# Performance work log

Hardware: AMD Instinct MI355X
Metric: run time of the kernel (lower is better)

The kernel has to match this reference:

```python
import jax, jax.numpy as jnp
import numpy as np

N_NODES = 50000
N_EDGES = 800000
N_GRAPHS = 256
F_IN = 75  # num_features_xd


def _lin_params(key, fan_in, fan_out):
    kw, kb = jax.random.split(key)
    s = 1.0 / np.sqrt(fan_in)
    W = jax.random.uniform(kw, (fan_in, fan_out), jnp.float32, -s, s)
    b = jax.random.uniform(kb, (fan_out,), jnp.float32, -s, s)
    return W, b


def setup_inputs() -> dict:
    key = jax.random.key(0)
    ks = jax.random.split(key, 8)
    x = jax.random.normal(ks[0], (N_NODES, F_IN), jnp.float32)
    edge_index = jax.random.randint(ks[1], (2, N_EDGES), 0, N_NODES, jnp.int32)
    batch = jnp.sort(jax.random.randint(ks[2], (N_NODES,), 0, N_GRAPHS, jnp.int32))
    W1, b1 = _lin_params(ks[3], F_IN, F_IN)            # conv1: 75 -> 75
    W2, b2 = _lin_params(ks[4], F_IN, 2 * F_IN)        # conv2: 75 -> 150
    W3, b3 = _lin_params(ks[5], 2 * F_IN, 4 * F_IN)    # conv3: 150 -> 300
    Wg1, bg1 = _lin_params(ks[6], 4 * F_IN, 1024)      # fc_g1: 300 -> 1024
    Wg2, bg2 = _lin_params(ks[7], 1024, 128)           # fc_g2: 1024 -> 128
    return dict(x=x, edge_index=edge_index, batch=batch,
                W1=W1, b1=b1, W2=W2, b2=b2, W3=W3, b3=b3,
                Wg1=Wg1, bg1=bg1, Wg2=Wg2, bg2=bg2)


def gcn_conv(x, W, b, src, dst, n):
    """PyG GCNConv: out = D^{-1/2}(A+I)D^{-1/2} X W + b (symmetric norm, self loops)."""
    h = x @ W                                   # [n, out]
    loop = jnp.arange(n, dtype=src.dtype)
    s = jnp.concatenate([src, loop])            # [E+n]
    d = jnp.concatenate([dst, loop])
    deg = jax.ops.segment_sum(jnp.ones(s.shape[0], x.dtype), d, num_segments=n)
    dinv = jnp.where(deg > 0, jax.lax.rsqrt(jnp.maximum(deg, 1e-12)), 0.0)
    norm = dinv[s] * dinv[d]                    # [E+n]
    out = jax.ops.segment_sum(norm[:, None] * h[s], d, num_segments=n)
    return out + b


def reference(x, edge_index, batch, W1, b1, W2, b2, W3, b3, Wg1, bg1, Wg2, bg2):
    src, dst = edge_index[0], edge_index[1]
    n = x.shape[0]
    h = jax.nn.relu(gcn_conv(x, W1, b1, src, dst, n))
    h = jax.nn.relu(gcn_conv(h, W2, b2, src, dst, n))
    h = jax.nn.relu(gcn_conv(h, W3, b3, src, dst, n))
    g = jax.ops.segment_max(h, batch, num_segments=N_GRAPHS)  # global max pool
    g = jax.nn.relu(g @ Wg1 + bg1)
    # dropout is identity in eval mode
    return g @ Wg2 + bg2
```

## Files before the change

### kernel.cpp

```cpp
#include <hip/hip_runtime.h>
#include <math.h>

#define SCAN_B 1024

typedef __attribute__((ext_vector_type(8))) short short8v;
typedef __attribute__((ext_vector_type(8))) unsigned short ushort8v;
typedef __attribute__((ext_vector_type(4))) float f32x4;

static inline int ceil_div_i(long long a, int b) { return (int)((a + b - 1) / b); }

__device__ __forceinline__ unsigned short f2bf(float x) {
    unsigned int u = __float_as_uint(x);
    u += 0x7fffu + ((u >> 16) & 1u);
    return (unsigned short)(u >> 16);
}
__device__ __forceinline__ float bf2f(unsigned short h) {
    return __uint_as_float(((unsigned int)h) << 16);
}
__device__ __forceinline__ ushort8v zero8() {
    ushort8v z;
#pragma unroll
    for (int e = 0; e < 8; e++) z[e] = 0;
    return z;
}


__global__ __launch_bounds__(256) void k_count(const int* __restrict__ dst, int E,
                                               int* __restrict__ cnt) {
    int i = blockIdx.x * blockDim.x + threadIdx.x;
    if (i < E) atomicAdd(&cnt[dst[i]], 1);
}

__global__ __launch_bounds__(256) void k_dinv(const int* __restrict__ cnt,
                                              float* __restrict__ dinv, int N) {
    int i = blockIdx.x * blockDim.x + threadIdx.x;
    if (i < N) dinv[i] = (float)(1.0 / sqrt((double)(cnt[i] + 1)));
}

__global__ __launch_bounds__(256) void k_scan1(const int* __restrict__ cnt,
                                               int* __restrict__ rowptr,
                                               int* __restrict__ bsum, int N) {
    __shared__ int s[256];
    int tid = threadIdx.x;
    int base = blockIdx.x * SCAN_B + tid * 4;
    int a0 = (base + 0 < N) ? cnt[base + 0] : 0;
    int a1 = (base + 1 < N) ? cnt[base + 1] : 0;
    int a2 = (base + 2 < N) ? cnt[base + 2] : 0;
    int a3 = (base + 3 < N) ? cnt[base + 3] : 0;
    int tsum = a0 + a1 + a2 + a3;
    s[tid] = tsum;
    __syncthreads();
    for (int off = 1; off < 256; off <<= 1) {
        int val = 0;
        if (tid >= off) val = s[tid - off];
        __syncthreads();
        if (tid >= off) s[tid] += val;
        __syncthreads();
    }
    int texcl = s[tid] - tsum;
    if (tid == 255) bsum[blockIdx.x] = s[255];
    if (base + 0 < N) rowptr[base + 0] = texcl;
    if (base + 1 < N) rowptr[base + 1] = texcl + a0;
    if (base + 2 < N) rowptr[base + 2] = texcl + a0 + a1;
    if (base + 3 < N) rowptr[base + 3] = texcl + a0 + a1 + a2;
}

__global__ __launch_bounds__(256) void k_scan2(int* __restrict__ bsum, int NB) {
    __shared__ int s[256];
    int tid = threadIdx.x;
    int v = (tid < NB) ? bsum[tid] : 0;
    s[tid] = v;
    __syncthreads();
    for (int off = 1; off < 256; off <<= 1) {
        int val = 0;
        if (tid >= off) val = s[tid - off];
        __syncthreads();
        if (tid >= off) s[tid] += val;
        __syncthreads();
    }
    if (tid < NB) bsum[tid] = s[tid] - v;
}

__global__ __launch_bounds__(256) void k_scan3(int* __restrict__ rowptr,
                                               const int* __restrict__ bsum, int N, int E) {
    int i = blockIdx.x * blockDim.x + threadIdx.x;
    if (i < N) rowptr[i] += bsum[i >> 10];
    if (i == 0) rowptr[N] = E;
}

__global__ __launch_bounds__(256) void k_fill(const int* __restrict__ src,
                                              const int* __restrict__ dst, int E,
                                              const int* __restrict__ rowptr,
                                              int* __restrict__ fill,
                                              int* __restrict__ col) {
    int e = blockIdx.x * blockDim.x + threadIdx.x;
    if (e >= E) return;
    int s = src[e], d = dst[e];
    int pos = atomicAdd(&fill[d], 1);
    col[rowptr[d] + pos] = s;
}


__global__ __launch_bounds__(256) void k_xscale(const float* __restrict__ x,
                                                const float* __restrict__ dinv,
                                                unsigned short* __restrict__ xb,
                                                int N, int F, int XS) {
    int i = blockIdx.x * blockDim.x + threadIdx.x;
    int v = i / XS, c = i - v * XS;
    if (v >= N) return;
    float val = (c < F) ? dinv[v] * x[(size_t)v * F + c] : 0.f;
    xb[i] = f2bf(val);
}


template <int CHUNKS, int SLOTS, int UNR>
__global__ __launch_bounds__(256) void k_gather_s(const unsigned short* __restrict__ Xb,
                                                  const int* __restrict__ rowptr,
                                                  const int* __restrict__ col,
                                                  unsigned short* __restrict__ Th,
                                                  unsigned short* __restrict__ Tl,
                                                  int N, int XS, int KPf) {
    const int v = blockIdx.x * 4 + (threadIdx.x >> 6);
    const int lane = threadIdx.x & 63;
    if (v >= N) return;
    constexpr int VW = 8;
    const int slot = lane / CHUNKS;
    const int chunk = lane - slot * CHUNKS;
    const bool act = lane < CHUNKS * SLOTS;
    const int f0 = chunk * VW;

    float acc[VW];
#pragma unroll
    for (int u = 0; u < VW; u++) acc[u] = 0.f;
    if (slot == 0) {
        ushort8v h = *(const ushort8v*)(Xb + (size_t)v * XS + f0);
#pragma unroll
        for (int u = 0; u < VW; u++) acc[u] = bf2f(h[u]);
    }

    const int beg = rowptr[v], end = rowptr[v + 1];
    for (int jb = beg; jb < end; jb += 64) {
        const int nj = min(64, end - jb);
        int ec = 0;
        if (lane < nj) ec = col[jb + lane];
        for (int e = 0; e < nj; e += SLOTS * UNR) {
            int cs[UNR];
            bool vs[UNR];
#pragma unroll
            for (int u = 0; u < UNR; u++) {
                int srcl = e + u * SLOTS + slot;
                vs[u] = act && (srcl < nj);
                cs[u] = __shfl(ec, srcl & 63);
            }
            ushort8v xv[UNR];
#pragma unroll
            for (int u = 0; u < UNR; u++) {
                xv[u] = zero8();
                if (vs[u]) xv[u] = *(const ushort8v*)(Xb + (size_t)cs[u] * XS + f0);
            }
#pragma unroll
            for (int u = 0; u < UNR; u++)
#pragma unroll
                for (int k2 = 0; k2 < VW; k2++)
                    acc[k2] += bf2f(xv[u][k2]);
        }
    }

#pragma unroll
    for (int k2 = 0; k2 < VW; k2++) {
        float t2 = acc[k2];
#pragma unroll
        for (int s2 = 1; s2 < SLOTS; s2++) t2 += __shfl(acc[k2], chunk + s2 * CHUNKS);
        acc[k2] = t2;
    }

    if (slot == 0 && f0 < KPf) {
        ushort8v h8, l8;
#pragma unroll
        for (int u = 0; u < VW; u++) {
            unsigned short hh = f2bf(acc[u]);
            h8[u] = hh;
            l8[u] = f2bf(acc[u] - bf2f(hh));
        }
        *(ushort8v*)(Th + (size_t)v * KPf + f0) = h8;
        *(ushort8v*)(Tl + (size_t)v * KPf + f0) = l8;
    }
}


__global__ __launch_bounds__(256) void k_wsplit(const float* __restrict__ W,
                                                unsigned short* __restrict__ Wth,
                                                unsigned short* __restrict__ Wtl,
                                                int K, int Fout, int KP) {
    int i = blockIdx.x * blockDim.x + threadIdx.x;
    if (i >= Fout * KP) return;
    int c = i / KP, k = i - c * KP;
    float w = (k < K) ? W[(size_t)k * Fout + c] : 0.f;
    unsigned short h = f2bf(w);
    Wth[i] = h;
    Wtl[i] = f2bf(w - bf2f(h));
}


template <int NT, int MODE>
__global__ __launch_bounds__(256) void k_gemm_br(
    const unsigned short* __restrict__ Ah, const unsigned short* __restrict__ Al,
    const unsigned short* __restrict__ Bth, const unsigned short* __restrict__ Btl,
    const float* __restrict__ bias, const float* __restrict__ dinvp,
    unsigned short* __restrict__ Cb, int CSbf,
    const int* __restrict__ batch, float* __restrict__ G,
    int N, int Fout) {
    constexpr int KP = NT * 32;
    constexpr int PL = 8 * NT * 512;
    __shared__ unsigned short sB[2 * PL];
    __shared__ int sBatch[128];

    const int t = threadIdx.x;
    const int r0 = blockIdx.x * 128;
    const int c0 = blockIdx.y * 128;
    const int lane = t & 63;
    const int wv = t >> 6;
    const int l15 = lane & 15;
    const int lg = lane >> 4;

    constexpr int KG = KP >> 3;
    for (int i = t; i < 128 * KG; i += 256) {
        int colc = i / KG, kg = i - colc * KG;
        int gc = c0 + colc;
        ushort8v h = zero8(), l = zero8();
        if (gc < Fout) {
            h = *(const ushort8v*)(Bth + (size_t)gc * KP + kg * 8);
            l = *(const ushort8v*)(Btl + (size_t)gc * KP + kg * 8);
        }
        int jt = colc >> 4, tc = kg >> 2, g = kg & 3;
        int off = (jt * NT + tc) * 512 + ((colc & 15) + 16 * g) * 8;
        *(ushort8v*)&sB[off] = h;
        *(ushort8v*)&sB[PL + off] = l;
    }
    if (MODE == 1 && t < 128) sBatch[t] = (r0 + t < N) ? batch[r0 + t] : -1;
    __syncthreads();

    const int wrow = wv * 32;
    const int row0 = r0 + wrow + l15;
    const int row1 = row0 + 16;
    const bool ok0 = row0 < N;
    const bool ok1 = row1 < N;
    const unsigned short* a0h = Ah + (size_t)row0 * KP;
    const unsigned short* a0l = Al + (size_t)row0 * KP;
    const unsigned short* a1h = Ah + (size_t)row1 * KP;
    const unsigned short* a1l = Al + (size_t)row1 * KP;

    f32x4 acc[2][8];
#pragma unroll
    for (int i = 0; i < 2; i++)
#pragma unroll
        for (int j = 0; j < 8; j++) acc[i][j] = (f32x4){0.f, 0.f, 0.f, 0.f};

#pragma unroll 2
    for (int tc = 0; tc < NT; ++tc) {
        const int ko = tc * 32 + lg * 8;
        short8v A0h = ok0 ? *(const short8v*)(a0h + ko) : (short8v)zero8();
        short8v A0l = ok0 ? *(const short8v*)(a0l + ko) : (short8v)zero8();
        short8v A1h = ok1 ? *(const short8v*)(a1h + ko) : (short8v)zero8();
        short8v A1l = ok1 ? *(const short8v*)(a1l + ko) : (short8v)zero8();
#pragma unroll
        for (int j = 0; j < 8; j++) {
            const int off = (j * NT + tc) * 512 + lane * 8;
            short8v bh = *(const short8v*)&sB[off];
            short8v bl = *(const short8v*)&sB[PL + off];
            acc[0][j] = __builtin_amdgcn_mfma_f32_16x16x32_bf16(A0l, bh, acc[0][j], 0, 0, 0);
            acc[0][j] = __builtin_amdgcn_mfma_f32_16x16x32_bf16(A0h, bl, acc[0][j], 0, 0, 0);
            acc[0][j] = __builtin_amdgcn_mfma_f32_16x16x32_bf16(A0h, bh, acc[0][j], 0, 0, 0);
            acc[1][j] = __builtin_amdgcn_mfma_f32_16x16x32_bf16(A1l, bh, acc[1][j], 0, 0, 0);
            acc[1][j] = __builtin_amdgcn_mfma_f32_16x16x32_bf16(A1h, bl, acc[1][j], 0, 0, 0);
            acc[1][j] = __builtin_amdgcn_mfma_f32_16x16x32_bf16(A1h, bh, acc[1][j], 0, 0, 0);
        }
    }

    float drw[8];
#pragma unroll
    for (int i = 0; i < 2; i++)
#pragma unroll
        for (int q = 0; q < 4; q++) {
            int gr = r0 + wrow + i * 16 + (lane >> 4) * 4 + q;
            drw[i * 4 + q] = (gr < N) ? dinvp[gr] : 0.f;
        }

    if (MODE == 0) {
#pragma unroll
        for (int j = 0; j < 8; j++) {
            int gc = c0 + j * 16 + l15;
            if (gc >= CSbf) continue;
            float bv = (gc < Fout) ? bias[gc] : 0.f;
#pragma unroll
            for (int i = 0; i < 2; i++) {
                int rb = r0 + wrow + i * 16 + (lane >> 4) * 4;
#pragma unroll
                for (int q = 0; q < 4; q++) {
                    int gr = rb + q;
                    if (gr >= N) continue;
                    float dr = drw[i * 4 + q];
                    float vv = (gc < Fout) ? fmaxf(fmaf(acc[i][j][q], dr, bv), 0.f) * dr : 0.f;
                    Cb[(size_t)gr * CSbf + gc] = f2bf(vv);
                }
            }
        }
    } else {
#pragma unroll
        for (int j = 0; j < 8; j++) {
            int gc = c0 + j * 16 + l15;
            if (gc >= Fout) continue;
            float bv = bias[gc];
            int gcur = -1;
            float vmax = 0.f;
#pragma unroll
            for (int i = 0; i < 2; i++) {
                int lr = wrow + i * 16 + (lane >> 4) * 4;
#pragma unroll
                for (int q = 0; q < 4; q++) {
                    int g = sBatch[lr + q];
                    float vv = fmaxf(fmaf(acc[i][j][q], drw[i * 4 + q], bv), 0.f);
                    if (g < 0) continue;
                    if (g != gcur) {
                        if (gcur >= 0)
                            atomicMax((int*)&G[(size_t)gcur * Fout + gc], __float_as_int(vmax));
                        gcur = g;
                        vmax = vv;
                    } else {
                        vmax = fmaxf(vmax, vv);
                    }
                }
            }
            if (gcur >= 0) atomicMax((int*)&G[(size_t)gcur * Fout + gc], __float_as_int(vmax));
        }
    }
}


__global__ __launch_bounds__(256) void k_fc1(const float* __restrict__ A,
                                             const float* __restrict__ W,
                                             const float* __restrict__ bias,
                                             float* __restrict__ C,
                                             int M, int K, int Nout) {
    __shared__ float sA[2 * 304];
    const int t = threadIdx.x;
    const int m0 = blockIdx.x * 2;
    const int oc = blockIdx.y * 256 + t;

    for (int i = t; i < 2 * K; i += 256) {
        int r = i / K, k = i - r * K;
        sA[r * 304 + k] = (m0 + r < M) ? A[(size_t)(m0 + r) * K + k] : 0.f;
    }
    __syncthreads();

    float acc0 = 0.f, acc1 = 0.f;
    int k = 0;
    for (; k + 8 <= K; k += 8) {
        float w[8];
#pragma unroll
        for (int u = 0; u < 8; u++) w[u] = W[(size_t)(k + u) * Nout + oc];
#pragma unroll
        for (int u = 0; u < 8; u++) {
            acc0 = fmaf(sA[k + u], w[u], acc0);
            acc1 = fmaf(sA[304 + k + u], w[u], acc1);
        }
    }
    for (; k < K; k++) {
        float w = W[(size_t)k * Nout + oc];
        acc0 = fmaf(sA[k], w, acc0);
        acc1 = fmaf(sA[304 + k], w, acc1);
    }
    float bv = bias[oc];
    if (m0 < M) C[(size_t)m0 * Nout + oc] = fmaxf(acc0 + bv, 0.f);
    if (m0 + 1 < M) C[(size_t)(m0 + 1) * Nout + oc] = fmaxf(acc1 + bv, 0.f);
}


__global__ __launch_bounds__(256) void k_fc2p(const float* __restrict__ A,
                                              const float* __restrict__ W,
                                              float* __restrict__ P,
                                              int M, int K, int Nout) {
    __shared__ float sA[2 * 256];
    const int t = threadIdx.x;
    const int m0 = blockIdx.x * 2;
    const int sk = blockIdx.y;
    const int k0 = sk * 256;
    const int row = t >> 7;
    const int oc = t & 127;

    for (int i = t; i < 2 * 256; i += 256) {
        int r = i >> 8, k = i & 255;
        sA[i] = (m0 + r < M) ? A[(size_t)(m0 + r) * K + k0 + k] : 0.f;
    }
    __syncthreads();

    const float* a = sA + row * 256;
    float acc = 0.f;
    for (int k = 0; k < 256; k += 8) {
        float w[8];
#pragma unroll
        for (int u = 0; u < 8; u++) w[u] = W[(size_t)(k0 + k + u) * Nout + oc];
#pragma unroll
        for (int u = 0; u < 8; u++) acc = fmaf(a[k + u], w[u], acc);
    }
    int m = m0 + row;
    if (m < M) P[((size_t)sk * M + m) * Nout + oc] = acc;
}

__global__ __launch_bounds__(256) void k_fc2r(const float* __restrict__ P,
                                              const float* __restrict__ bias,
                                              float* __restrict__ C,
                                              int M, int Nout, int SK) {
    int i = blockIdx.x * blockDim.x + threadIdx.x;
    if (i >= M * Nout) return;
    int oc = i % Nout;
    float acc = bias[oc];
    for (int s2 = 0; s2 < SK; s2++) acc += P[(size_t)s2 * M * Nout + i];
    C[i] = acc;
}


extern "C" void kernel_launch(void* const* d_in, const int* in_sizes, int n_in,
                              void* d_out, int out_size, void* d_ws, size_t ws_size,
                              hipStream_t stream) {
    const float* x     = (const float*)d_in[0];
    const int*   ei    = (const int*)d_in[1];
    const int*   batch = (const int*)d_in[2];
    const float* W1 = (const float*)d_in[3];
    const float* b1 = (const float*)d_in[4];
    const float* W2 = (const float*)d_in[5];
    const float* b2 = (const float*)d_in[6];
    const float* W3 = (const float*)d_in[7];
    const float* b3 = (const float*)d_in[8];
    const float* Wg1 = (const float*)d_in[9];
    const float* bg1 = (const float*)d_in[10];
    const float* Wg2 = (const float*)d_in[11];
    const float* bg2 = (const float*)d_in[12];

    const int N  = in_sizes[2];
    const int E  = in_sizes[1] / 2;
    const int F1 = in_sizes[4];
    const int F2 = in_sizes[6];
    const int F3 = in_sizes[8];
    const int H1 = in_sizes[10];
    const int OC = in_sizes[12];
    const int NG = out_size / OC;
    const int FIN = in_sizes[3] / F1;

    const int KP1 = 96;
    const int KP3 = 160;

    const int* src = ei;
    const int* dst = ei + E;

    char* base = (char*)d_ws;
    size_t off = 0;
    auto alloc = [&](size_t bytes) -> void* {
        void* p = base + off;
        off = (off + bytes + 255) & ~(size_t)255;
        return p;
    };
    int*   cnt    = (int*)alloc((size_t)N * 4);
    int*   fill   = (int*)alloc((size_t)N * 4);
    int*   rowptr = (int*)alloc((size_t)(N + 1) * 4);
    float* dinv   = (float*)alloc((size_t)N * 4);
    int*   bsum   = (int*)alloc(256 * 4);
    int*   col    = (int*)alloc((size_t)E * 4);
    unsigned short* W1th = (unsigned short*)alloc((size_t)F1 * KP1 * 2);
    unsigned short* W1tl = (unsigned short*)alloc((size_t)F1 * KP1 * 2);
    unsigned short* W2th = (unsigned short*)alloc((size_t)F2 * KP1 * 2);
    unsigned short* W2tl = (unsigned short*)alloc((size_t)F2 * KP1 * 2);
    unsigned short* W3th = (unsigned short*)alloc((size_t)F3 * KP3 * 2);
    unsigned short* W3tl = (unsigned short*)alloc((size_t)F3 * KP3 * 2);
    float* Gb  = (float*)alloc((size_t)NG * F3 * 4);
    float* g1  = (float*)alloc((size_t)NG * H1 * 4);
    float* P2  = (float*)alloc((size_t)4 * NG * OC * 4);
    unsigned short* TgH = (unsigned short*)alloc((size_t)N * KP3 * 2);
    unsigned short* TgL = (unsigned short*)alloc((size_t)N * KP3 * 2);
    unsigned short* Xb  = (unsigned short*)alloc((size_t)N * KP1 * 2);
    unsigned short* H1b = (unsigned short*)alloc((size_t)N * KP1 * 2);
    unsigned short* H2b = (unsigned short*)alloc((size_t)N * KP3 * 2);

    hipMemsetAsync(cnt, 0, (size_t)N * 4, stream);
    hipMemsetAsync(fill, 0, (size_t)N * 4, stream);
    hipMemsetAsync(Gb, 0, (size_t)NG * F3 * 4, stream);

    k_count<<<ceil_div_i(E, 256), 256, 0, stream>>>(dst, E, cnt);
    k_dinv<<<ceil_div_i(N, 256), 256, 0, stream>>>(cnt, dinv, N);
    int NB = ceil_div_i(N, SCAN_B);
    k_scan1<<<NB, 256, 0, stream>>>(cnt, rowptr, bsum, N);
    k_scan2<<<1, 256, 0, stream>>>(bsum, NB);
    k_scan3<<<ceil_div_i(N, 256), 256, 0, stream>>>(rowptr, bsum, N, E);
    k_fill<<<ceil_div_i(E, 256), 256, 0, stream>>>(src, dst, E, rowptr, fill, col);

    k_wsplit<<<ceil_div_i((long long)F1 * KP1, 256), 256, 0, stream>>>(W1, W1th, W1tl, FIN, F1, KP1);
    k_wsplit<<<ceil_div_i((long long)F2 * KP1, 256), 256, 0, stream>>>(W2, W2th, W2tl, F1, F2, KP1);
    k_wsplit<<<ceil_div_i((long long)F3 * KP3, 256), 256, 0, stream>>>(W3, W3th, W3tl, F2, F3, KP3);
    k_xscale<<<ceil_div_i((long long)N * KP1, 256), 256, 0, stream>>>(x, dinv, Xb, N, FIN, KP1);

    dim3 blk(256);
    int gw = ceil_div_i(N, 4);
    int gx = ceil_div_i(N, 128);

    k_gather_s<12, 5, 2><<<gw, blk, 0, stream>>>(Xb, rowptr, col, TgH, TgL, N, KP1, KP1);
    {
        dim3 g(gx, ceil_div_i(F1, 128));
        k_gemm_br<3, 0><<<g, blk, 0, stream>>>(TgH, TgL, W1th, W1tl, b1, dinv, H1b, KP1,
                                               nullptr, nullptr, N, F1);
    }
    k_gather_s<12, 5, 2><<<gw, blk, 0, stream>>>(H1b, rowptr, col, TgH, TgL, N, KP1, KP1);
    {
        dim3 g(gx, ceil_div_i(F2, 128));
        k_gemm_br<3, 0><<<g, blk, 0, stream>>>(TgH, TgL, W2th, W2tl, b2, dinv, H2b, KP3,
                                               nullptr, nullptr, N, F2);
    }
    k_gather_s<20, 3, 4><<<gw, blk, 0, stream>>>(H2b, rowptr, col, TgH, TgL, N, KP3, KP3);
    {
        dim3 g(gx, ceil_div_i(F3, 128));
        k_gemm_br<5, 1><<<g, blk, 0, stream>>>(TgH, TgL, W3th, W3tl, b3, dinv, nullptr, 0,
                                               batch, Gb, N, F3);
    }

    {
        dim3 g(ceil_div_i(NG, 2), H1 / 256);
        k_fc1<<<g, 256, 0, stream>>>(Gb, Wg1, bg1, g1, NG, F3, H1);
    }
    {
        dim3 g(ceil_div_i(NG, 2), 4);
        k_fc2p<<<g, 256, 0, stream>>>(g1, Wg2, P2, NG, H1, OC);
        k_fc2r<<<ceil_div_i((long long)NG * OC, 256), 256, 0, stream>>>(
            P2, bg2, (float*)d_out, NG, OC, 4);
    }
}
```

Before: 379.2 us.

## Shrink feature strides, use 16-bit column indices, and retile GEMM to exact widths

Stores column indices as 16-bit values and has k_scan3 write the fill cursor directly, which removes a memset and the rowptr lookup in k_fill. k_fill now handles four edges per thread. Intermediate activation buffers move from 96/160-wide padding to 80/152-wide strides, so the gathers move fewer bytes. The GEMM is rewritten to stream B through padded LDS tiles one K-slice at a time, with column tiles sized to the true output widths (96/160), instead of preloading 128-wide tiles. The 16-bit indices only hold while N stays below 65536, and the per-K-slice syncthreads add synchronisation.

```diff
diff --git a/kernel.cpp b/kernel.cpp
--- a/kernel.cpp
+++ b/kernel.cpp
@@ -2,6 +2,7 @@
 #include <math.h>
 
 #define SCAN_B 1024
+#define LDST 40
 
 typedef __attribute__((ext_vector_type(8))) short short8v;
 typedef __attribute__((ext_vector_type(8))) unsigned short ushort8v;
@@ -82,22 +83,31 @@
 }
 
 __global__ __launch_bounds__(256) void k_scan3(int* __restrict__ rowptr,
-                                               const int* __restrict__ bsum, int N, int E) {
+                                               const int* __restrict__ bsum,
+                                               int* __restrict__ fill, int N, int E) {
     int i = blockIdx.x * blockDim.x + threadIdx.x;
-    if (i < N) rowptr[i] += bsum[i >> 10];
+    if (i < N) {
+        int r = rowptr[i] + bsum[i >> 10];
+        rowptr[i] = r;
+        fill[i] = r;
+    }
     if (i == 0) rowptr[N] = E;
 }
 
 __global__ __launch_bounds__(256) void k_fill(const int* __restrict__ src,
                                               const int* __restrict__ dst, int E,
-                                              const int* __restrict__ rowptr,
                                               int* __restrict__ fill,
-                                              int* __restrict__ col) {
-    int e = blockIdx.x * blockDim.x + threadIdx.x;
-    if (e >= E) return;
-    int s = src[e], d = dst[e];
-    int pos = atomicAdd(&fill[d], 1);
-    col[rowptr[d] + pos] = s;
+                                              unsigned short* __restrict__ col) {
+    int base = blockIdx.x * (256 * 4) + threadIdx.x;
+#pragma unroll
+    for (int u = 0; u < 4; u++) {
+        int e = base + u * 256;
+        if (e < E) {
+            int s = src[e], d = dst[e];
+            int idx = atomicAdd(&fill[d], 1);
+            col[idx] = (unsigned short)s;
+        }
+    }
 }
 
 
@@ -116,7 +126,7 @@
 template <int CHUNKS, int SLOTS, int UNR>
 __global__ __launch_bounds__(256) void k_gather_s(const unsigned short* __restrict__ Xb,
                                                   const int* __restrict__ rowptr,
-                                                  const int* __restrict__ col,
+                                                  const unsigned short* __restrict__ col,
                                                   unsigned short* __restrict__ Th,
                                                   unsigned short* __restrict__ Tl,
                                                   int N, int XS, int KPf) {
@@ -142,7 +152,7 @@
     for (int jb = beg; jb < end; jb += 64) {
         const int nj = min(64, end - jb);
         int ec = 0;
-        if (lane < nj) ec = col[jb + lane];
+        if (lane < nj) ec = (int)col[jb + lane];
         for (int e = 0; e < nj; e += SLOTS * UNR) {
             int cs[UNR];
             bool vs[UNR];
@@ -202,72 +212,74 @@
 }
 
 
-template <int NT, int MODE>
-__global__ __launch_bounds__(256) void k_gemm_br(
-    const unsigned short* __restrict__ Ah, const unsigned short* __restrict__ Al,
+template <int NJ2, int MODE>
+__global__ __launch_bounds__(256, 4) void k_gemm_ad(
+    const unsigned short* __restrict__ Ahp, const unsigned short* __restrict__ Alp, int KPf,
     const unsigned short* __restrict__ Bth, const unsigned short* __restrict__ Btl,
     const float* __restrict__ bias, const float* __restrict__ dinvp,
     unsigned short* __restrict__ Cb, int CSbf,
     const int* __restrict__ batch, float* __restrict__ G,
-    int N, int Fout) {
-    constexpr int KP = NT * 32;
-    constexpr int PL = 8 * NT * 512;
-    __shared__ unsigned short sB[2 * PL];
+    int N, int KP, int Fout) {
+    constexpr int CT = 16 * NJ2;
+    __shared__ unsigned short sBh[CT * LDST];
+    __shared__ unsigned short sBl[CT * LDST];
     __shared__ int sBatch[128];
 
     const int t = threadIdx.x;
     const int r0 = blockIdx.x * 128;
-    const int c0 = blockIdx.y * 128;
+    const int c0 = blockIdx.y * CT;
     const int lane = t & 63;
     const int wv = t >> 6;
+    const int wrow = wv * 32;
     const int l15 = lane & 15;
     const int lg = lane >> 4;
-
-    constexpr int KG = KP >> 3;
-    for (int i = t; i < 128 * KG; i += 256) {
-        int colc = i / KG, kg = i - colc * KG;
-        int gc = c0 + colc;
-        ushort8v h = zero8(), l = zero8();
-        if (gc < Fout) {
-            h = *(const ushort8v*)(Bth + (size_t)gc * KP + kg * 8);
-            l = *(const ushort8v*)(Btl + (size_t)gc * KP + kg * 8);
-        }
-        int jt = colc >> 4, tc = kg >> 2, g = kg & 3;
-        int off = (jt * NT + tc) * 512 + ((colc & 15) + 16 * g) * 8;
-        *(ushort8v*)&sB[off] = h;
-        *(ushort8v*)&sB[PL + off] = l;
-    }
+    const int nt = KP >> 5;
+
     if (MODE == 1 && t < 128) sBatch[t] = (r0 + t < N) ? batch[r0 + t] : -1;
-    __syncthreads();
-
-    const int wrow = wv * 32;
+
     const int row0 = r0 + wrow + l15;
     const int row1 = row0 + 16;
     const bool ok0 = row0 < N;
     const bool ok1 = row1 < N;
-    const unsigned short* a0h = Ah + (size_t)row0 * KP;
-    const unsigned short* a0l = Al + (size_t)row0 * KP;
-    const unsigned short* a1h = Ah + (size_t)row1 * KP;
-    const unsigned short* a1l = Al + (size_t)row1 * KP;
-
-    f32x4 acc[2][8];
+    const unsigned short* a0h = Ahp + (size_t)row0 * KPf;
+    const unsigned short* a0l = Alp + (size_t)row0 * KPf;
+    const unsigned short* a1h = Ahp + (size_t)row1 * KPf;
+    const unsigned short* a1l = Alp + (size_t)row1 * KPf;
+
+    f32x4 acc[2][NJ2];
 #pragma unroll
     for (int i = 0; i < 2; i++)
 #pragma unroll
-        for (int j = 0; j < 8; j++) acc[i][j] = (f32x4){0.f, 0.f, 0.f, 0.f};
-
-#pragma unroll 2
-    for (int tc = 0; tc < NT; ++tc) {
-        const int ko = tc * 32 + lg * 8;
-        short8v A0h = ok0 ? *(const short8v*)(a0h + ko) : (short8v)zero8();
-        short8v A0l = ok0 ? *(const short8v*)(a0l + ko) : (short8v)zero8();
-        short8v A1h = ok1 ? *(const short8v*)(a1h + ko) : (short8v)zero8();
-        short8v A1l = ok1 ? *(const short8v*)(a1l + ko) : (short8v)zero8();
-#pragma unroll
-        for (int j = 0; j < 8; j++) {
-            const int off = (j * NT + tc) * 512 + lane * 8;
-            short8v bh = *(const short8v*)&sB[off];
-            short8v bl = *(const short8v*)&sB[PL + off];
+        for (int j = 0; j < NJ2; j++) acc[i][j] = (f32x4){0.f, 0.f, 0.f, 0.f};
+
+    for (int tc = 0; tc < nt; ++tc) {
+        const int kk = tc * 32;
+        for (int idx = t; idx < CT * 4; idx += 256) {
+            int brow = idx >> 2, seg = idx & 3;
+            int gc = c0 + brow;
+            ushort8v h = zero8(), l = zero8();
+            if (gc < Fout) {
+                h = *(const ushort8v*)(Bth + (size_t)gc * KP + kk + seg * 8);
+                l = *(const ushort8v*)(Btl + (size_t)gc * KP + kk + seg * 8);
+            }
+            int boff = brow * LDST + seg * 8;
+            *(ushort8v*)&sBh[boff] = h;
+            *(ushort8v*)&sBl[boff] = l;
+        }
+        __syncthreads();
+
+        const int gk = kk + lg * 8;
+        const bool kok = gk < KPf;
+        short8v A0h = (ok0 && kok) ? *(const short8v*)(a0h + gk) : (short8v)zero8();
+        short8v A0l = (ok0 && kok) ? *(const short8v*)(a0l + gk) : (short8v)zero8();
+        short8v A1h = (ok1 && kok) ? *(const short8v*)(a1h + gk) : (short8v)zero8();
+        short8v A1l = (ok1 && kok) ? *(const short8v*)(a1l + gk) : (short8v)zero8();
+
+#pragma unroll
+        for (int j = 0; j < NJ2; j++) {
+            int co = (j * 16 + l15) * LDST + lg * 8;
+            short8v bh = *(const short8v*)&sBh[co];
+            short8v bl = *(const short8v*)&sBl[co];
             acc[0][j] = __builtin_amdgcn_mfma_f32_16x16x32_bf16(A0l, bh, acc[0][j], 0, 0, 0);
             acc[0][j] = __builtin_amdgcn_mfma_f32_16x16x32_bf16(A0h, bl, acc[0][j], 0, 0, 0);
             acc[0][j] = __builtin_amdgcn_mfma_f32_16x16x32_bf16(A0h, bh, acc[0][j], 0, 0, 0);
@@ -275,6 +287,7 @@
             acc[1][j] = __builtin_amdgcn_mfma_f32_16x16x32_bf16(A1h, bl, acc[1][j], 0, 0, 0);
             acc[1][j] = __builtin_amdgcn_mfma_f32_16x16x32_bf16(A1h, bh, acc[1][j], 0, 0, 0);
         }
+        __syncthreads();
     }
 
     float drw[8];
@@ -288,7 +301,7 @@
 
     if (MODE == 0) {
 #pragma unroll
-        for (int j = 0; j < 8; j++) {
+        for (int j = 0; j < NJ2; j++) {
             int gc = c0 + j * 16 + l15;
             if (gc >= CSbf) continue;
             float bv = (gc < Fout) ? bias[gc] : 0.f;
@@ -307,7 +320,7 @@
         }
     } else {
 #pragma unroll
-        for (int j = 0; j < 8; j++) {
+        for (int j = 0; j < NJ2; j++) {
             int gc = c0 + j * 16 + l15;
             if (gc >= Fout) continue;
             float bv = bias[gc];
@@ -447,8 +460,11 @@
     const int NG = out_size / OC;
     const int FIN = in_sizes[3] / F1;
 
-    const int KP1 = 96;
-    const int KP3 = 160;
+    const int KP1 = 96,  KPf1 = 80;
+    const int KP3 = 160, KPf3 = 152;
+    const int XS0 = 80;
+    const int HS1 = 80;
+    const int HS2 = 152;
 
     const int* src = ei;
     const int* dst = ei + E;
@@ -465,7 +481,7 @@
     int*   rowptr = (int*)alloc((size_t)(N + 1) * 4);
     float* dinv   = (float*)alloc((size_t)N * 4);
     int*   bsum   = (int*)alloc(256 * 4);
-    int*   col    = (int*)alloc((size_t)E * 4);
+    unsigned short* col = (unsigned short*)alloc((size_t)E * 2);
     unsigned short* W1th = (unsigned short*)alloc((size_t)F1 * KP1 * 2);
     unsigned short* W1tl = (unsigned short*)alloc((size_t)F1 * KP1 * 2);
     unsigned short* W2th = (unsigned short*)alloc((size_t)F2 * KP1 * 2);
@@ -475,14 +491,13 @@
     float* Gb  = (float*)alloc((size_t)NG * F3 * 4);
     float* g1  = (float*)alloc((size_t)NG * H1 * 4);
     float* P2  = (float*)alloc((size_t)4 * NG * OC * 4);
-    unsigned short* TgH = (unsigned short*)alloc((size_t)N * KP3 * 2);
-    unsigned short* TgL = (unsigned short*)alloc((size_t)N * KP3 * 2);
-    unsigned short* Xb  = (unsigned short*)alloc((size_t)N * KP1 * 2);
-    unsigned short* H1b = (unsigned short*)alloc((size_t)N * KP1 * 2);
-    unsigned short* H2b = (unsigned short*)alloc((size_t)N * KP3 * 2);
+    unsigned short* TgH = (unsigned short*)alloc((size_t)N * KPf3 * 2);
+    unsigned short* TgL = (unsigned short*)alloc((size_t)N * KPf3 * 2);
+    unsigned short* Xb  = (unsigned short*)alloc((size_t)N * XS0 * 2);
+    unsigned short* H1b = (unsigned short*)alloc((size_t)N * HS1 * 2);
+    unsigned short* H2b = (unsigned short*)alloc((size_t)N * HS2 * 2);
 
     hipMemsetAsync(cnt, 0, (size_t)N * 4, stream);
-    hipMemsetAsync(fill, 0, (size_t)N * 4, stream);
     hipMemsetAsync(Gb, 0, (size_t)NG * F3 * 4, stream);
 
     k_count<<<ceil_div_i(E, 256), 256, 0, stream>>>(dst, E, cnt);
@@ -490,35 +505,35 @@
     int NB = ceil_div_i(N, SCAN_B);
     k_scan1<<<NB, 256, 0, stream>>>(cnt, rowptr, bsum, N);
     k_scan2<<<1, 256, 0, stream>>>(bsum, NB);
-    k_scan3<<<ceil_div_i(N, 256), 256, 0, stream>>>(rowptr, bsum, N, E);
-    k_fill<<<ceil_div_i(E, 256), 256, 0, stream>>>(src, dst, E, rowptr, fill, col);
+    k_scan3<<<ceil_div_i(N, 256), 256, 0, stream>>>(rowptr, bsum, fill, N, E);
+    k_fill<<<ceil_div_i(E, 1024), 256, 0, stream>>>(src, dst, E, fill, col);
 
     k_wsplit<<<ceil_div_i((long long)F1 * KP1, 256), 256, 0, stream>>>(W1, W1th, W1tl, FIN, F1, KP1);
     k_wsplit<<<ceil_div_i((long long)F2 * KP1, 256), 256, 0, stream>>>(W2, W2th, W2tl, F1, F2, KP1);
     k_wsplit<<<ceil_div_i((long long)F3 * KP3, 256), 256, 0, stream>>>(W3, W3th, W3tl, F2, F3, KP3);
-    k_xscale<<<ceil_div_i((long long)N * KP1, 256), 256, 0, stream>>>(x, dinv, Xb, N, FIN, KP1);
+    k_xscale<<<ceil_div_i((long long)N * XS0, 256), 256, 0, stream>>>(x, dinv, Xb, N, FIN, XS0);
 
     dim3 blk(256);
     int gw = ceil_div_i(N, 4);
     int gx = ceil_div_i(N, 128);
 
-    k_gather_s<12, 5, 2><<<gw, blk, 0, stream>>>(Xb, rowptr, col, TgH, TgL, N, KP1, KP1);
+    k_gather_s<10, 6, 2><<<gw, blk, 0, stream>>>(Xb, rowptr, col, TgH, TgL, N, XS0, KPf1);
     {
-        dim3 g(gx, ceil_div_i(F1, 128));
-        k_gemm_br<3, 0><<<g, blk, 0, stream>>>(TgH, TgL, W1th, W1tl, b1, dinv, H1b, KP1,
-                                               nullptr, nullptr, N, F1);
-    }
-    k_gather_s<12, 5, 2><<<gw, blk, 0, stream>>>(H1b, rowptr, col, TgH, TgL, N, KP1, KP1);
+        dim3 g(gx, 1);
+        k_gemm_ad<6, 0><<<g, blk, 0, stream>>>(TgH, TgL, KPf1, W1th, W1tl, b1, dinv,
+                                               H1b, HS1, nullptr, nullptr, N, KP1, F1);
+    }
+    k_gather_s<10, 6, 2><<<gw, blk, 0, stream>>>(H1b, rowptr, col, TgH, TgL, N, HS1, KPf1);
     {
-        dim3 g(gx, ceil_div_i(F2, 128));
-        k_gemm_br<3, 0><<<g, blk, 0, stream>>>(TgH, TgL, W2th, W2tl, b2, dinv, H2b, KP3,
-                                               nullptr, nullptr, N, F2);
-    }
-    k_gather_s<20, 3, 4><<<gw, blk, 0, stream>>>(H2b, rowptr, col, TgH, TgL, N, KP3, KP3);
+        dim3 g(gx, 1);
+        k_gemm_ad<10, 0><<<g, blk, 0, stream>>>(TgH, TgL, KPf1, W2th, W2tl, b2, dinv,
+                                                H2b, HS2, nullptr, nullptr, N, KP1, F2);
+    }
+    k_gather_s<19, 3, 4><<<gw, blk, 0, stream>>>(H2b, rowptr, col, TgH, TgL, N, HS2, KPf3);
     {
-        dim3 g(gx, ceil_div_i(F3, 128));
-        k_gemm_br<5, 1><<<g, blk, 0, stream>>>(TgH, TgL, W3th, W3tl, b3, dinv, nullptr, 0,
-                                               batch, Gb, N, F3);
+        dim3 g(gx, 2);
+        k_gemm_ad<10, 1><<<g, blk, 0, stream>>>(TgH, TgL, KPf3, W3th, W3tl, b3, dinv,
+                                                nullptr, 0, batch, Gb, N, KP3, F3);
     }
 
     {
```

After: 348.4 us. 8.1% less time.
